# Kernel optimization log

Hardware: AMD Instinct MI355X
Metric: run time of the kernel (lower is better)

## Reference

```python
import jax, jax.numpy as jnp
import numpy as np

IN_FEATURES = 4096
OUT_FEATURES = 4096
PACKED_IN = (IN_FEATURES + 3) // 4  # 1024


def _unpack_ternary(packed, scale, original_in_features):
    # packed: (O, P) uint8; each byte holds 4 two-bit fields encoding {-1,0,+1} as {0,1,2}
    p = packed.astype(jnp.uint8)
    fields = jnp.stack(
        [p & 3, (p >> 2) & 3, (p >> 4) & 3, (p >> 6) & 3], axis=-1
    )  # (O, P, 4)
    unpacked = fields.reshape(packed.shape[0], -1)[:, :original_in_features]
    decoded = unpacked.astype(scale.dtype) - 1.0  # back to {-1,0,+1}
    return decoded * scale  # per-output-channel scale, (O, IN)


def setup_inputs() -> dict:
    key = jax.random.key(0)
    k_x, k_w, k_s, k_b = jax.random.split(key, 4)
    x = jax.random.normal(k_x, (4, 2048, IN_FEATURES), dtype=jnp.float32)
    # sample ternary codes {0,1,2} per 2-bit field, then pack 4 per byte
    fields = jax.random.randint(k_w, (OUT_FEATURES, PACKED_IN, 4), 0, 3).astype(jnp.uint8)
    packed_weight = (
        fields[..., 0]
        | (fields[..., 1] << 2)
        | (fields[..., 2] << 4)
        | (fields[..., 3] << 6)
    )  # (O, P) uint8
    scale = jax.random.uniform(k_s, (OUT_FEATURES, 1), dtype=jnp.float32, minval=0.01, maxval=0.1)
    bias = jax.random.normal(k_b, (OUT_FEATURES,), dtype=jnp.float32)
    return {"x": x, "packed_weight": packed_weight, "scale": scale, "bias": bias}


def reference(x, packed_weight, scale, bias):
    weight = _unpack_ternary(packed_weight, scale, IN_FEATURES)  # (O, IN) fp32
    # F.linear: x @ W.T + b
    return jnp.einsum("bsi,oi->bso", x, weight) + bias
```

## Files before the change

### kernel.cpp

```cpp
#include <hip/hip_runtime.h>
#include <hip/hip_bf16.h>
#include <stdint.h>

#define M_TOT 8192
#define N_TOT 4096
#define K_TOT 4096
#define PACKED_K 1024

typedef __attribute__((ext_vector_type(4))) float f32x4;
typedef __attribute__((ext_vector_type(4))) int i32x4;
typedef __attribute__((ext_vector_type(16))) int i32x16;
typedef __attribute__((ext_vector_type(4))) unsigned int u32x4;

typedef const __attribute__((address_space(1))) void* gas_cptr;
typedef __attribute__((address_space(3))) void* las_ptr;

#define SX (6.0f / 127.0f)
#define SX_INV (127.0f / 6.0f)

__device__ __forceinline__ void gload_lds16(const void* g, void* l) {
    __builtin_amdgcn_global_load_lds((gas_cptr)g, (las_ptr)l, 16, 0, 0);
}

__global__ void detect_i32(const uint32_t* __restrict__ pw, uint32_t* __restrict__ flag) {
    unsigned long long big = __ballot(pw[threadIdx.x & 63] > 255u);
    if (threadIdx.x == 0) *flag = (big == 0ull) ? 1u : 0u;
}


__device__ __forceinline__ uint32_t q8pack(f32x4 v) {
    int a = (int)rintf(fminf(fmaxf(v.x * SX_INV, -127.f), 127.f));
    int b = (int)rintf(fminf(fmaxf(v.y * SX_INV, -127.f), 127.f));
    int c = (int)rintf(fminf(fmaxf(v.z * SX_INV, -127.f), 127.f));
    int d = (int)rintf(fminf(fmaxf(v.w * SX_INV, -127.f), 127.f));
    return (uint32_t)(a & 0xFF) | ((uint32_t)(b & 0xFF) << 8)
         | ((uint32_t)(c & 0xFF) << 16) | ((uint32_t)(d & 0xFF) << 24);
}

__global__ void quant_x_tiled(const float* __restrict__ x,
                              int8_t* __restrict__ aq, int ngran) {
    int stride = gridDim.x * blockDim.x;
    for (int g = blockIdx.x * blockDim.x + threadIdx.x; g < ngran; g += stride) {
        const int mb = g >> 16;
        const int w16 = g & 65535;
        const int kt = w16 >> 10;
        const int w = w16 & 1023;
        const int kstep = w >> 9;
        const int rb = (w >> 6) & 7;
        const int kslot = (w >> 5) & 1;
        const int rl = w & 31;
        const int row = mb * 256 + rb * 32 + rl;
        const int col = kt * 64 + kstep * 32 + kslot * 16;
        const f32x4* src = (const f32x4*)(x + (size_t)row * K_TOT + col);
        uint32_t w0 = q8pack(src[0]);
        uint32_t w1 = q8pack(src[1]);
        uint32_t w2 = q8pack(src[2]);
        uint32_t w3 = q8pack(src[3]);
        *(u32x4*)(aq + (size_t)g * 16) = (u32x4){w0, w1, w2, w3};
    }
}

__global__ void unpack_w_tiled(const uint8_t* __restrict__ pw,
                               int8_t* __restrict__ bq,
                               const uint32_t* __restrict__ flag, int ngran) {
    const uint32_t i32mode = *flag;
    int stride = gridDim.x * blockDim.x;
    for (int g = blockIdx.x * blockDim.x + threadIdx.x; g < ngran; g += stride) {
        const int nb = g >> 16;
        const int w16 = g & 65535;
        const int kt = w16 >> 10;
        const int w = w16 & 1023;
        const int kstep = w >> 9;
        const int rb = (w >> 6) & 7;
        const int kslot = (w >> 5) & 1;
        const int rl = w & 31;
        const int row = nb * 256 + rb * 32 + rl;
        const int pidx = row * PACKED_K + kt * 16 + kstep * 8 + kslot * 4;
        uint32_t p;
        if (i32mode) {
            const uint32_t* p32 = (const uint32_t*)pw;
            uint32_t b0 = p32[pidx + 0] & 0xFFu;
            uint32_t b1 = p32[pidx + 1] & 0xFFu;
            uint32_t b2 = p32[pidx + 2] & 0xFFu;
            uint32_t b3 = p32[pidx + 3] & 0xFFu;
            p = b0 | (b1 << 8) | (b2 << 16) | (b3 << 24);
        } else {
            p = *(const uint32_t*)(pw + pidx);
        }
        uint32_t o[4];
#pragma unroll
        for (int i = 0; i < 4; ++i) {
            uint32_t b = (p >> (8 * i)) & 0xFFu;
            uint32_t f0 = b & 3u, f1 = (b >> 2) & 3u, f2 = (b >> 4) & 3u, f3 = b >> 6;
            o[i] = ((f0 - 1u) & 0xFFu) | (((f1 - 1u) & 0xFFu) << 8)
                 | (((f2 - 1u) & 0xFFu) << 16) | (((f3 - 1u) & 0xFFu) << 24);
        }
        *(u32x4*)(bq + (size_t)g * 16) = (u32x4){o[0], o[1], o[2], o[3]};
    }
}

__global__ __launch_bounds__(512, 2) void gemm_tern_i8(
        const int8_t* __restrict__ Aq,
        const int8_t* __restrict__ Bq,
        const float* __restrict__ scale,
        const float* __restrict__ bias,
        float* __restrict__ out) {
    __shared__ uint8_t ldsA[32768];

    const int tid  = threadIdx.x;
    const int lane = tid & 63;
    const int wid  = tid >> 6;
    const int wm   = wid >> 2;
    const int wn   = wid & 3;

    const int wg  = blockIdx.x;
    const int cpx = gridDim.x >> 3;
    const int swz = (wg & 7) * cpx + (wg >> 3);
    const int mblk = swz >> 4;
    const int nblk = swz & 15;
    const int m0  = mblk * 256;
    const int n0  = nblk * 256;

    const int8_t* Abase = Aq + (size_t)mblk * 1048576;
    const int8_t* Bbase = Bq + (size_t)nblk * 1048576;
    const i32x4*  Bb4   = (const i32x4*)(Bbase + wn * 2048 + (lane << 4));

#define STAGE_A(t, db) do {                                                           \
        const int8_t* sa = Abase + (size_t)(t) * 16384 + (tid << 4);                  \
        gload_lds16(sa,        ldsA + (db) * 16384 + (tid << 4));                     \
        gload_lds16(sa + 8192, ldsA + (db) * 16384 + 8192 + (tid << 4));              \
    } while (0)

#define LOADB(r00, r10, r01, r11, t) do {                                             \
        const i32x4* pb = Bb4 + (size_t)(t) * 1024;                                   \
        r00 = pb[0]; r10 = pb[64]; r01 = pb[512]; r11 = pb[576];                      \
    } while (0)

#define RD_A(mf, ks, db) (*(const i32x4*)(ldsA + (db) * 16384 + (ks) * 8192          \
                              + (wm * 4 + (mf)) * 1024 + (lane << 4)))

#define BAR()        __builtin_amdgcn_s_barrier()
#define SCHEDBAR()   __builtin_amdgcn_sched_barrier(0)
#define WAIT_LGKM4() asm volatile("s_waitcnt lgkmcnt(4)" ::: "memory")
#define WAIT_LGKM0() asm volatile("s_waitcnt lgkmcnt(0)" ::: "memory")
#define WAIT_VM0()   asm volatile("s_waitcnt vmcnt(0)" ::: "memory")

#define MFMA_I8(a, b, c) __builtin_amdgcn_mfma_i32_32x32x32_i8(a, b, c, 0, 0, 0)

#define KTILE(t, DB, Bc00, Bc10, Bc01, Bc11, Bn00, Bn10, Bn01, Bn11)                  \
    if ((t) + 1 < NT) {                                                               \
        STAGE_A((t) + 1, 1 - (DB));                                                   \
        LOADB(Bn00, Bn10, Bn01, Bn11, (t) + 1);                                       \
    }                                                                                 \
    a0k0 = RD_A(0, 0, DB); a1k0 = RD_A(1, 0, DB);                                     \
    a2k0 = RD_A(2, 0, DB); a3k0 = RD_A(3, 0, DB);                                     \
    a0k1 = RD_A(0, 1, DB); a1k1 = RD_A(1, 1, DB);                                     \
    a2k1 = RD_A(2, 1, DB); a3k1 = RD_A(3, 1, DB);                                     \
    WAIT_LGKM4(); SCHEDBAR();                                                         \
    __builtin_amdgcn_s_setprio(1);                                                    \
    acc00 = MFMA_I8(a0k0, Bc00, acc00);  acc01 = MFMA_I8(a0k0, Bc10, acc01);          \
    acc10 = MFMA_I8(a1k0, Bc00, acc10);  acc11 = MFMA_I8(a1k0, Bc10, acc11);          \
    acc20 = MFMA_I8(a2k0, Bc00, acc20);  acc21 = MFMA_I8(a2k0, Bc10, acc21);          \
    acc30 = MFMA_I8(a3k0, Bc00, acc30);  acc31 = MFMA_I8(a3k0, Bc10, acc31);          \
    __builtin_amdgcn_s_setprio(0);                                                    \
    WAIT_LGKM0(); SCHEDBAR();                                                         \
    __builtin_amdgcn_s_setprio(1);                                                    \
    acc00 = MFMA_I8(a0k1, Bc01, acc00);  acc01 = MFMA_I8(a0k1, Bc11, acc01);          \
    acc10 = MFMA_I8(a1k1, Bc01, acc10);  acc11 = MFMA_I8(a1k1, Bc11, acc11);          \
    acc20 = MFMA_I8(a2k1, Bc01, acc20);  acc21 = MFMA_I8(a2k1, Bc11, acc21);          \
    acc30 = MFMA_I8(a3k1, Bc01, acc30);  acc31 = MFMA_I8(a3k1, Bc11, acc31);          \
    __builtin_amdgcn_s_setprio(0);                                                    \
    WAIT_VM0();                                                                       \
    BAR();

    i32x16 acc00 = {0}, acc01 = {0}, acc10 = {0}, acc11 = {0};
    i32x16 acc20 = {0}, acc21 = {0}, acc30 = {0}, acc31 = {0};
#pragma unroll
    for (int j = 0; j < 16; ++j) {
        acc00[j] = 0; acc01[j] = 0; acc10[j] = 0; acc11[j] = 0;
        acc20[j] = 0; acc21[j] = 0; acc30[j] = 0; acc31[j] = 0;
    }

    const int NT = K_TOT / 64;

    i32x4 Bx00, Bx10, Bx01, Bx11, By00, By10, By01, By11;

    STAGE_A(0, 0);
    LOADB(Bx00, Bx10, Bx01, Bx11, 0);
    WAIT_VM0();
    BAR();

    i32x4 a0k0, a1k0, a2k0, a3k0;
    i32x4 a0k1, a1k1, a2k1, a3k1;

    for (int t = 0; t < NT; t += 2) {
        KTILE(t,     0, Bx00, Bx10, Bx01, Bx11, By00, By10, By01, By11);
        KTILE(t + 1, 1, By00, By10, By01, By11, Bx00, Bx10, Bx01, Bx11);
    }

    const int rl    = lane & 31;
    const int rbase = (lane >> 5) << 2;
#pragma unroll
    for (int nf = 0; nf < 2; ++nf) {
        const int col = n0 + wn * 64 + nf * 32 + rl;
        const float fs = SX * scale[col];
        const float bv = bias[col];
#pragma unroll
        for (int mf = 0; mf < 4; ++mf) {
            const i32x16 a = (mf == 0) ? (nf == 0 ? acc00 : acc01)
                           : (mf == 1) ? (nf == 0 ? acc10 : acc11)
                           : (mf == 2) ? (nf == 0 ? acc20 : acc21)
                                       : (nf == 0 ? acc30 : acc31);
#pragma unroll
            for (int j = 0; j < 16; ++j) {
                const int row = m0 + wm * 128 + mf * 32 + (j & 3) + 8 * (j >> 2) + rbase;
                out[(size_t)row * N_TOT + col] = (float)a[j] * fs + bv;
            }
        }
    }
#undef STAGE_A
#undef LOADB
#undef RD_A
#undef BAR
#undef SCHEDBAR
#undef WAIT_LGKM4
#undef WAIT_LGKM0
#undef WAIT_VM0
#undef MFMA_I8
#undef KTILE
}

__global__ void naive_tern(const float* __restrict__ x,
                           const uint8_t* __restrict__ pw,
                           const float* __restrict__ scale,
                           const float* __restrict__ bias,
                           float* __restrict__ out) {
    const int n = blockIdx.x * blockDim.x + threadIdx.x;
    const int m = blockIdx.y;
    const uint32_t* p32 = (const uint32_t*)pw;
    bool i32mode = true;
    for (int i = 0; i < 64; ++i)
        if (p32[i] > 255u) { i32mode = false; break; }
    const float* xr = x + (size_t)m * K_TOT;
    float acc = 0.f;
    if (i32mode) {
        const uint32_t* wr = p32 + (size_t)n * PACKED_K;
        for (int p = 0; p < PACKED_K; ++p) {
            uint32_t b = wr[p] & 0xFFu;
            acc += xr[4 * p + 0] * (float)((int)(b & 3u) - 1);
            acc += xr[4 * p + 1] * (float)((int)((b >> 2) & 3u) - 1);
            acc += xr[4 * p + 2] * (float)((int)((b >> 4) & 3u) - 1);
            acc += xr[4 * p + 3] * (float)((int)((b >> 6) & 3u) - 1);
        }
    } else {
        const uint8_t* wr = pw + (size_t)n * PACKED_K;
        for (int p = 0; p < PACKED_K; ++p) {
            uint32_t b = wr[p];
            acc += xr[4 * p + 0] * (float)((int)(b & 3u) - 1);
            acc += xr[4 * p + 1] * (float)((int)((b >> 2) & 3u) - 1);
            acc += xr[4 * p + 2] * (float)((int)((b >> 4) & 3u) - 1);
            acc += xr[4 * p + 3] * (float)((int)((b >> 6) & 3u) - 1);
        }
    }
    out[(size_t)m * N_TOT + n] = acc * scale[n] + bias[n];
}

extern "C" void kernel_launch(void* const* d_in, const int* in_sizes, int n_in,
                              void* d_out, int out_size, void* d_ws, size_t ws_size,
                              hipStream_t stream) {
    const float*   x     = (const float*)d_in[0];
    const uint8_t* pw    = (const uint8_t*)d_in[1];
    const float*   scale = (const float*)d_in[2];
    const float*   bias  = (const float*)d_in[3];
    float*         out   = (float*)d_out;

    const size_t A_BYTES = (size_t)M_TOT * K_TOT;
    const size_t B_BYTES = (size_t)N_TOT * K_TOT;
    const size_t NEED    = A_BYTES + B_BYTES + 64;

    if (ws_size >= NEED) {
        int8_t*   Aq   = (int8_t*)d_ws;
        int8_t*   Bq   = (int8_t*)((uint8_t*)d_ws + A_BYTES);
        uint32_t* flag = (uint32_t*)((uint8_t*)d_ws + A_BYTES + B_BYTES);
        detect_i32<<<1, 64, 0, stream>>>((const uint32_t*)pw, flag);
        unpack_w_tiled<<<2048, 256, 0, stream>>>(pw, Bq, flag, (int)(B_BYTES / 16));
        quant_x_tiled<<<2048, 256, 0, stream>>>(x, Aq, (int)(A_BYTES / 16));
        gemm_tern_i8<<<(M_TOT / 256) * (N_TOT / 256), 512, 0, stream>>>(Aq, Bq, scale, bias, out);
    } else {
        dim3 grid(N_TOT / 256, M_TOT);
        naive_tern<<<grid, 256, 0, stream>>>(x, pw, scale, bias, out);
    }
}
```

Before: 202.5 us.

## Deepen A staging to a 4-slot LDS ring and prefetch A fragments

The shared-memory A buffer grows from 2 to 4 slots, so global-to-LDS loads are issued three tiles ahead. Waits switch to partial vmcnt so the newest tile load can stay in flight across the barrier. The next tile's A fragments are read from LDS into a second register set while the current tile's MFMAs run, replacing the old split wait between the two k-halves. The main loop is unrolled with a peeled tail. This costs double the LDS per block and extra VGPRs for the second fragment set, which may cause spills or lower occupancy.

```diff
diff --git a/kernel.cpp b/kernel.cpp
--- a/kernel.cpp
+++ b/kernel.cpp
@@ -105,7 +105,7 @@
         const float* __restrict__ scale,
         const float* __restrict__ bias,
         float* __restrict__ out) {
-    __shared__ uint8_t ldsA[32768];
+    __shared__ uint8_t lds[65536];
 
     const int tid  = threadIdx.x;
     const int lane = tid & 63;
@@ -127,8 +127,9 @@
 
 #define STAGE_A(t, db) do {                                                           \
         const int8_t* sa = Abase + (size_t)(t) * 16384 + (tid << 4);                  \
-        gload_lds16(sa,        ldsA + (db) * 16384 + (tid << 4));                     \
-        gload_lds16(sa + 8192, ldsA + (db) * 16384 + 8192 + (tid << 4));              \
+        uint8_t* la = lds + (db) * 16384 + (tid << 4);                                \
+        gload_lds16(sa,        la);                                                   \
+        gload_lds16(sa + 8192, la + 8192);                                            \
     } while (0)
 
 #define LOADB(r00, r10, r01, r11, t) do {                                             \
@@ -136,41 +137,41 @@
         r00 = pb[0]; r10 = pb[64]; r01 = pb[512]; r11 = pb[576];                      \
     } while (0)
 
-#define RD_A(mf, ks, db) (*(const i32x4*)(ldsA + (db) * 16384 + (ks) * 8192          \
+#define RD_A(mf, ks, db) (*(const i32x4*)(lds + (db) * 16384 + (ks) * 8192           \
                               + (wm * 4 + (mf)) * 1024 + (lane << 4)))
+
+#define READ8(F, RDB) do {                                                            \
+        F[0] = RD_A(0, 0, RDB); F[2] = RD_A(1, 0, RDB);                               \
+        F[4] = RD_A(2, 0, RDB); F[6] = RD_A(3, 0, RDB);                               \
+        F[1] = RD_A(0, 1, RDB); F[3] = RD_A(1, 1, RDB);                               \
+        F[5] = RD_A(2, 1, RDB); F[7] = RD_A(3, 1, RDB);                               \
+    } while (0)
 
 #define BAR()        __builtin_amdgcn_s_barrier()
 #define SCHEDBAR()   __builtin_amdgcn_sched_barrier(0)
-#define WAIT_LGKM4() asm volatile("s_waitcnt lgkmcnt(4)" ::: "memory")
-#define WAIT_LGKM0() asm volatile("s_waitcnt lgkmcnt(0)" ::: "memory")
-#define WAIT_VM0()   asm volatile("s_waitcnt vmcnt(0)" ::: "memory")
+#define WAIT_LGKM(N) asm volatile("s_waitcnt lgkmcnt(" #N ")" ::: "memory")
+#define WAIT_VM(N)   asm volatile("s_waitcnt vmcnt(" #N ")" ::: "memory")
 
 #define MFMA_I8(a, b, c) __builtin_amdgcn_mfma_i32_32x32x32_i8(a, b, c, 0, 0, 0)
 
-#define KTILE(t, DB, Bc00, Bc10, Bc01, Bc11, Bn00, Bn10, Bn01, Bn11)                  \
-    if ((t) + 1 < NT) {                                                               \
-        STAGE_A((t) + 1, 1 - (DB));                                                   \
-        LOADB(Bn00, Bn10, Bn01, Bn11, (t) + 1);                                       \
-    }                                                                                 \
-    a0k0 = RD_A(0, 0, DB); a1k0 = RD_A(1, 0, DB);                                     \
-    a2k0 = RD_A(2, 0, DB); a3k0 = RD_A(3, 0, DB);                                     \
-    a0k1 = RD_A(0, 1, DB); a1k1 = RD_A(1, 1, DB);                                     \
-    a2k1 = RD_A(2, 1, DB); a3k1 = RD_A(3, 1, DB);                                     \
-    WAIT_LGKM4(); SCHEDBAR();                                                         \
+#define KTILE(t, CUR, NXT, Bc00, Bc10, Bc01, Bc11, Bn00, Bn10, Bn01, Bn11,            \
+              DO_RD, DO_STAGE, DO_LOADB, VMC)                                         \
+    if (DO_RD) READ8(NXT, ((t) + 1) & 3);                                             \
+    if (DO_LOADB) LOADB(Bn00, Bn10, Bn01, Bn11, (t) + 1);                             \
+    if (DO_STAGE) STAGE_A((t) + 3, ((t) + 3) & 3);                                    \
+    if (DO_RD) { WAIT_LGKM(8); } else { WAIT_LGKM(0); }                               \
+    SCHEDBAR();                                                                       \
     __builtin_amdgcn_s_setprio(1);                                                    \
-    acc00 = MFMA_I8(a0k0, Bc00, acc00);  acc01 = MFMA_I8(a0k0, Bc10, acc01);          \
-    acc10 = MFMA_I8(a1k0, Bc00, acc10);  acc11 = MFMA_I8(a1k0, Bc10, acc11);          \
-    acc20 = MFMA_I8(a2k0, Bc00, acc20);  acc21 = MFMA_I8(a2k0, Bc10, acc21);          \
-    acc30 = MFMA_I8(a3k0, Bc00, acc30);  acc31 = MFMA_I8(a3k0, Bc10, acc31);          \
+    acc00 = MFMA_I8(CUR[0], Bc00, acc00);  acc01 = MFMA_I8(CUR[0], Bc10, acc01);      \
+    acc10 = MFMA_I8(CUR[2], Bc00, acc10);  acc11 = MFMA_I8(CUR[2], Bc10, acc11);      \
+    acc20 = MFMA_I8(CUR[4], Bc00, acc20);  acc21 = MFMA_I8(CUR[4], Bc10, acc21);      \
+    acc30 = MFMA_I8(CUR[6], Bc00, acc30);  acc31 = MFMA_I8(CUR[6], Bc10, acc31);      \
+    acc00 = MFMA_I8(CUR[1], Bc01, acc00);  acc01 = MFMA_I8(CUR[1], Bc11, acc01);      \
+    acc10 = MFMA_I8(CUR[3], Bc01, acc10);  acc11 = MFMA_I8(CUR[3], Bc11, acc11);      \
+    acc20 = MFMA_I8(CUR[5], Bc01, acc20);  acc21 = MFMA_I8(CUR[5], Bc11, acc21);      \
+    acc30 = MFMA_I8(CUR[7], Bc01, acc30);  acc31 = MFMA_I8(CUR[7], Bc11, acc31);      \
     __builtin_amdgcn_s_setprio(0);                                                    \
-    WAIT_LGKM0(); SCHEDBAR();                                                         \
-    __builtin_amdgcn_s_setprio(1);                                                    \
-    acc00 = MFMA_I8(a0k1, Bc01, acc00);  acc01 = MFMA_I8(a0k1, Bc11, acc01);          \
-    acc10 = MFMA_I8(a1k1, Bc01, acc10);  acc11 = MFMA_I8(a1k1, Bc11, acc11);          \
-    acc20 = MFMA_I8(a2k1, Bc01, acc20);  acc21 = MFMA_I8(a2k1, Bc11, acc21);          \
-    acc30 = MFMA_I8(a3k1, Bc01, acc30);  acc31 = MFMA_I8(a3k1, Bc11, acc31);          \
-    __builtin_amdgcn_s_setprio(0);                                                    \
-    WAIT_VM0();                                                                       \
+    WAIT_VM(VMC); SCHEDBAR();                                                         \
     BAR();
 
     i32x16 acc00 = {0}, acc01 = {0}, acc10 = {0}, acc11 = {0};
@@ -181,22 +182,32 @@
         acc20[j] = 0; acc21[j] = 0; acc30[j] = 0; acc31[j] = 0;
     }
 
-    const int NT = K_TOT / 64;
-
-    i32x4 Bx00, Bx10, Bx01, Bx11, By00, By10, By01, By11;
-
+    i32x4 BX00, BX10, BX01, BX11, BY00, BY10, BY01, BY11;
+
+    LOADB(BX00, BX10, BX01, BX11, 0);
     STAGE_A(0, 0);
-    LOADB(Bx00, Bx10, Bx01, Bx11, 0);
-    WAIT_VM0();
+    STAGE_A(1, 1);
+    STAGE_A(2, 2);
+    WAIT_VM(2); SCHEDBAR();
     BAR();
 
-    i32x4 a0k0, a1k0, a2k0, a3k0;
-    i32x4 a0k1, a1k1, a2k1, a3k1;
-
-    for (int t = 0; t < NT; t += 2) {
-        KTILE(t,     0, Bx00, Bx10, Bx01, Bx11, By00, By10, By01, By11);
-        KTILE(t + 1, 1, By00, By10, By01, By11, Bx00, Bx10, Bx01, Bx11);
-    }
+    i32x4 fA[8], fB[8];
+    READ8(fA, 0);
+
+    for (int t = 0; t < 56; t += 4) {
+        KTILE(t,     fA, fB, BX00, BX10, BX01, BX11, BY00, BY10, BY01, BY11, 1, 1, 1, 2);
+        KTILE(t + 1, fB, fA, BY00, BY10, BY01, BY11, BX00, BX10, BX01, BX11, 1, 1, 1, 2);
+        KTILE(t + 2, fA, fB, BX00, BX10, BX01, BX11, BY00, BY10, BY01, BY11, 1, 1, 1, 2);
+        KTILE(t + 3, fB, fA, BY00, BY10, BY01, BY11, BX00, BX10, BX01, BX11, 1, 1, 1, 2);
+    }
+    KTILE(56, fA, fB, BX00, BX10, BX01, BX11, BY00, BY10, BY01, BY11, 1, 1, 1, 2);
+    KTILE(57, fB, fA, BY00, BY10, BY01, BY11, BX00, BX10, BX01, BX11, 1, 1, 1, 2);
+    KTILE(58, fA, fB, BX00, BX10, BX01, BX11, BY00, BY10, BY01, BY11, 1, 1, 1, 2);
+    KTILE(59, fB, fA, BY00, BY10, BY01, BY11, BX00, BX10, BX01, BX11, 1, 1, 1, 2);
+    KTILE(60, fA, fB, BX00, BX10, BX01, BX11, BY00, BY10, BY01, BY11, 1, 1, 1, 2);
+    KTILE(61, fB, fA, BY00, BY10, BY01, BY11, BX00, BX10, BX01, BX11, 1, 0, 1, 0);
+    KTILE(62, fA, fB, BX00, BX10, BX01, BX11, BY00, BY10, BY01, BY11, 1, 0, 1, 0);
+    KTILE(63, fB, fA, BY00, BY10, BY01, BY11, BX00, BX10, BX01, BX11, 0, 0, 0, 0);
 
     const int rl    = lane & 31;
     const int rbase = (lane >> 5) << 2;
@@ -221,11 +232,11 @@
 #undef STAGE_A
 #undef LOADB
 #undef RD_A
+#undef READ8
 #undef BAR
 #undef SCHEDBAR
-#undef WAIT_LGKM4
-#undef WAIT_LGKM0
-#undef WAIT_VM0
+#undef WAIT_LGKM
+#undef WAIT_VM
 #undef MFMA_I8
 #undef KTILE
 }
```

Measured after the change: 203.2 us. About the same (+0.3%).
